# Optimization experiments

Hardware: AMD Instinct MI355X
Metric: run time of the kernel (lower is better)

Reference implementation:

```python
import jax, jax.numpy as jnp
import numpy as np

MODES = 16
WIDTH = 64
DEPTH = 4
MLP = 128


def spectral_conv(x, w_cplx):
    # x: [B, C, H, W] float32; w_cplx: [C, C, m1, m2] complex64
    B, C, H, W = x.shape
    x_ft = jnp.fft.rfft2(x)  # [B, C, H, W//2+1] complex
    m1, m2 = MODES, MODES
    low = jnp.einsum('bixy,ioxy->boxy', x_ft[:, :, :m1, :m2], w_cplx)
    out_ft = jnp.zeros((B, C, H, W // 2 + 1), dtype=jnp.complex64)
    out_ft = out_ft.at[:, :, :m1, :m2].set(low)
    return jnp.fft.irfft2(out_ft, s=(H, W)).astype(x.dtype)


def conv1x1(x, w, b):
    # x: [B,Cin,H,W], w: [Cout,Cin], b: [Cout]
    return jnp.einsum('bihw,oi->bohw', x, w) + b[None, :, None, None]


def setup_inputs() -> dict:
    key = jax.random.key(0)
    ks = jax.random.split(key, 4 + 4 * DEPTH)
    inp = {}
    inp['x'] = jax.random.normal(ks[0], (8, 3, 256, 256), dtype=jnp.float32)
    inp['fc0_w'] = jax.random.normal(ks[1], (WIDTH, 3), dtype=jnp.float32) * 0.1
    inp['fc0_b'] = jnp.zeros((WIDTH,), dtype=jnp.float32)
    scale = 1.0 / (WIDTH * WIDTH)
    sw_re, sw_im, ww, wb = [], [], [], []
    for i in range(DEPTH):
        k1, k2, k3 = jax.random.split(ks[4 + i], 3)
        sw_re.append(scale * jax.random.uniform(k1, (WIDTH, WIDTH, MODES, MODES), dtype=jnp.float32))
        sw_im.append(scale * jax.random.uniform(k2, (WIDTH, WIDTH, MODES, MODES), dtype=jnp.float32))
        ww.append(jax.random.normal(k3, (WIDTH, WIDTH), dtype=jnp.float32) * 0.05)
        wb.append(jnp.zeros((WIDTH,), dtype=jnp.float32))
    inp['spec_w_re'] = jnp.stack(sw_re)  # [D, C, C, m1, m2]
    inp['spec_w_im'] = jnp.stack(sw_im)
    inp['w_w'] = jnp.stack(ww)           # [D, C, C]
    inp['w_b'] = jnp.stack(wb)           # [D, C]
    inp['fc1_w'] = jax.random.normal(ks[2], (MLP, WIDTH), dtype=jnp.float32) * 0.05
    inp['fc1_b'] = jnp.zeros((MLP,), dtype=jnp.float32)
    inp['fc2_w'] = jax.random.normal(ks[3], (3, MLP), dtype=jnp.float32) * 0.05
    inp['fc2_b'] = jnp.zeros((3,), dtype=jnp.float32)
    return inp


def reference(x, fc0_w, fc0_b, spec_w_re, spec_w_im, w_w, w_b, fc1_w, fc1_b, fc2_w, fc2_b):
    # Dropout is identity in eval mode.
    h = conv1x1(x, fc0_w, fc0_b)  # [B, WIDTH, H, W]
    for i in range(DEPTH):
        w_cplx = spec_w_re[i] + 1j * spec_w_im[i]
        x1 = spectral_conv(h, w_cplx)
        x2 = conv1x1(h, w_w[i], w_b[i])
        h = jax.nn.relu(x1 + x2)
    h = jnp.transpose(h, (0, 2, 3, 1))  # [B, H, W, WIDTH]
    h = jax.nn.relu(jnp.einsum('bhwc,mc->bhwm', h, fc1_w) + fc1_b)
    h = jnp.einsum('bhwm,om->bhwo', h, fc2_w) + fc2_b
    return jnp.transpose(h, (0, 3, 1, 2))  # [B, 3, H, W]
```

## Files before the change

### kernel.cpp

```cpp
#include <hip/hip_runtime.h>

#define Hd 256
#define Wd 256
#define HW 65536
#define C 64
#define B 8
#define M 16
#define NDEPTH 4
#define NMLP 128

typedef __attribute__((ext_vector_type(8))) __bf16 bf16x8;
typedef __attribute__((ext_vector_type(4))) float f32x4;

__device__ inline void bar_lgkm() {
    asm volatile("s_waitcnt lgkmcnt(0)" ::: "memory");
    __builtin_amdgcn_s_barrier();
}

__device__ inline void split_pack8(const float* v, uint4& hq, uint4& lq) {
    unsigned hw[4], lw[4];
#pragma unroll
    for (int i = 0; i < 4; ++i) {
        float a = v[2 * i], bb = v[2 * i + 1];
        unsigned ua = __float_as_uint(a);
        unsigned ha = (ua + 0x7fffu + ((ua >> 16) & 1u)) & 0xffff0000u;
        float ra = a - __uint_as_float(ha);
        unsigned ural = __float_as_uint(ra);
        unsigned la = (ural + 0x7fffu + ((ural >> 16) & 1u)) >> 16;
        unsigned ub = __float_as_uint(bb);
        unsigned hb = (ub + 0x7fffu + ((ub >> 16) & 1u)) & 0xffff0000u;
        float rb = bb - __uint_as_float(hb);
        unsigned urbl = __float_as_uint(rb);
        unsigned lb = (urbl + 0x7fffu + ((urbl >> 16) & 1u)) >> 16;
        hw[i] = (ha >> 16) | (hb & 0xffff0000u);
        lw[i] = la | (lb << 16);
    }
    hq = make_uint4(hw[0], hw[1], hw[2], hw[3]);
    lq = make_uint4(lw[0], lw[1], lw[2], lw[3]);
}

__device__ inline void split1(float s, ushort& h, ushort& l) {
    unsigned ua = __float_as_uint(s);
    unsigned ha = (ua + 0x7fffu + ((ua >> 16) & 1u)) & 0xffff0000u;
    float r = s - __uint_as_float(ha);
    unsigned ur = __float_as_uint(r);
    h = (ushort)(ha >> 16);
    l = (ushort)((ur + 0x7fffu + ((ur >> 16) & 1u)) >> 16);
}

__device__ inline uint4 pack8(const unsigned* v) {
    uint4 r;
    r.x = v[0] | (v[1] << 16);
    r.y = v[2] | (v[3] << 16);
    r.z = v[4] | (v[5] << 16);
    r.w = v[6] | (v[7] << 16);
    return r;
}


__global__ void k_table(float2* __restrict__ tab) {
    int t = threadIdx.x;
    double a = (6.283185307179586476925286766559 / 256.0) * (double)t;
    tab[t] = make_float2((float)cos(a), (float)sin(a));
}

__global__ void k_prep0(const float2* __restrict__ tab, const float* __restrict__ fc1w,
                        const float* __restrict__ ww, float* __restrict__ trig,
                        uint4* __restrict__ trigs_h, uint4* __restrict__ trigs_l,
                        uint4* __restrict__ wws_h, uint4* __restrict__ wws_l,
                        uint4* __restrict__ w1s_h, uint4* __restrict__ w1s_l) {
    int blk = blockIdx.x, t = threadIdx.x;
    if (blk < 32) {
        int k = blk & 15;
        float2 e = tab[(k * t) & 255];
        trig[blk * 256 + t] = (blk < 16) ? e.x : e.y;
    } else if (blk < 36) {
        int idx = (blk - 32) * 256 + t;
        int kc = idx >> 8, x = idx & 255;
        float v[8];
#pragma unroll
        for (int j = 0; j < 8; ++j) {
            int row = kc * 8 + j;
            float2 e = tab[((row & 15) * x) & 255];
            v[j] = (row < 16) ? e.x : e.y;
        }
        uint4 hq, lq; split_pack8(v, hq, lq);
        trigs_h[idx] = hq; trigs_l[idx] = lq;
    } else if (blk < 44) {
        int idx = (blk - 36) * 256 + t;
        int o = idx & 63, kc = (idx >> 6) & 3, ph = (idx >> 8) & 1, d = idx >> 9;
        float v[8];
#pragma unroll
        for (int j = 0; j < 8; ++j)
            v[j] = ww[d * 4096 + o * 64 + ph * 32 + kc * 8 + j];
        uint4 hq, lq; split_pack8(v, hq, lq);
        wws_h[idx] = hq; wws_l[idx] = lq;
    } else {
        int idx = (blk - 44) * 256 + t;
        int m = idx & 127, kc = (idx >> 7) & 3, ph = idx >> 9;
        float v[8];
#pragma unroll
        for (int j = 0; j < 8; ++j)
            v[j] = fc1w[m * 64 + ph * 32 + kc * 8 + j];
        uint4 hq, lq; split_pack8(v, hq, lq);
        w1s_h[idx] = hq; w1s_l[idx] = lq;
    }
}

__global__ void k_prep_et(const float2* __restrict__ tab,
                          uint4* __restrict__ ETh, uint4* __restrict__ ETl) {
    int c = blockIdx.x * 256 + threadIdx.x;
    if (c >= 1024) return;
    int ph = c >> 7, kc = (c >> 5) & 3, m = c & 31;
    float v[8];
#pragma unroll
    for (int j = 0; j < 8; ++j) {
        int y = ph * 32 + kc * 8 + j;
        float2 e = tab[((m & 15) * y) & 255];
        v[j] = (m < 16) ? e.x : -e.y;
    }
    uint4 hq, lq;
    split_pack8(v, hq, lq);
    ETh[c] = hq; ETl[c] = lq;
}

__global__ void k_fc0(const float* __restrict__ x, const float* __restrict__ w,
                      const float* __restrict__ bias,
                      ushort* __restrict__ hs_h, ushort* __restrict__ hs_l) {
    int gp = blockIdx.x * 256 + threadIdx.x;
    int b = gp >> 13, pg = gp & 8191;
    int pix0 = pg * 8;
    float xv[3][8];
#pragma unroll
    for (int ch = 0; ch < 3; ++ch) {
        float4 a = *(const float4*)(x + (size_t)(b * 3 + ch) * HW + pix0);
        float4 c4 = *(const float4*)(x + (size_t)(b * 3 + ch) * HW + pix0 + 4);
        xv[ch][0] = a.x; xv[ch][1] = a.y; xv[ch][2] = a.z; xv[ch][3] = a.w;
        xv[ch][4] = c4.x; xv[ch][5] = c4.y; xv[ch][6] = c4.z; xv[ch][7] = c4.w;
    }
    for (int o = 0; o < C; ++o) {
        float w0 = w[o * 3 + 0], w1 = w[o * 3 + 1], w2 = w[o * 3 + 2], bv = bias[o];
        float v[8];
#pragma unroll
        for (int j = 0; j < 8; ++j)
            v[j] = fmaf(w0, xv[0][j], fmaf(w1, xv[1][j], fmaf(w2, xv[2][j], bv)));
        uint4 hq, lq; split_pack8(v, hq, lq);
        *(uint4*)(hs_h + (size_t)(b * 64 + o) * HW + pix0) = hq;
        *(uint4*)(hs_l + (size_t)(b * 64 + o) * HW + pix0) = lq;
    }
}

__global__ __launch_bounds__(256, 4)
void k_fwd_y(const ushort* __restrict__ hs_h, const ushort* __restrict__ hs_l,
             const uint4* __restrict__ ETh, const uint4* __restrict__ ETl,
             float* __restrict__ T1F) {
    int blk = blockIdx.x;
    int xh = blk & 1, bc = blk >> 1;
    int x0 = xh * 128;
    int t = threadIdx.x;
    int w = t >> 6, l = t & 63;
    int lr = l & 15, lq = l >> 4;
    const ushort* pH = hs_h + (size_t)bc * HW + x0 + w * 32 + lr;
    const ushort* pL = hs_l + (size_t)bc * HW + x0 + w * 32 + lr;
    f32x4 acc[2][2];
#pragma unroll
    for (int u = 0; u < 2; ++u)
#pragma unroll
        for (int xt = 0; xt < 2; ++xt) {
            acc[u][xt][0] = 0.f; acc[u][xt][1] = 0.f;
            acc[u][xt][2] = 0.f; acc[u][xt][3] = 0.f;
        }
    unsigned h0[2][8], l0[2][8], h1[2][8], l1[2][8];
    auto loadp = [&](unsigned hv[2][8], unsigned lv[2][8], int ph) {
#pragma unroll
        for (int xt = 0; xt < 2; ++xt)
#pragma unroll
            for (int j = 0; j < 8; ++j) {
                int off = (ph * 32 + lq * 8 + j) * 256 + xt * 16;
                hv[xt][j] = pH[off];
                lv[xt][j] = pL[off];
            }
    };
    loadp(h0, l0, 0);
#pragma unroll
    for (int ph = 0; ph < 8; ++ph) {
        unsigned (*ch)[8] = (ph & 1) ? h1 : h0;
        unsigned (*cl)[8] = (ph & 1) ? l1 : l0;
        unsigned (*nh)[8] = (ph & 1) ? h0 : h1;
        unsigned (*nl)[8] = (ph & 1) ? l0 : l1;
        if (ph < 7) loadp(nh, nl, ph + 1);
        bf16x8 Ah[2], Al[2];
#pragma unroll
        for (int u = 0; u < 2; ++u) {
            int ci = ph * 128 + lq * 32 + u * 16 + lr;
            Ah[u] = __builtin_bit_cast(bf16x8, ETh[ci]);
            Al[u] = __builtin_bit_cast(bf16x8, ETl[ci]);
        }
#pragma unroll
        for (int xt = 0; xt < 2; ++xt) {
            bf16x8 Bh = __builtin_bit_cast(bf16x8, pack8(ch[xt]));
            bf16x8 Bl = __builtin_bit_cast(bf16x8, pack8(cl[xt]));
#pragma unroll
            for (int u = 0; u < 2; ++u) {
                acc[u][xt] = __builtin_amdgcn_mfma_f32_16x16x32_bf16(Ah[u], Bh, acc[u][xt], 0, 0, 0);
                acc[u][xt] = __builtin_amdgcn_mfma_f32_16x16x32_bf16(Ah[u], Bl, acc[u][xt], 0, 0, 0);
                acc[u][xt] = __builtin_amdgcn_mfma_f32_16x16x32_bf16(Al[u], Bh, acc[u][xt], 0, 0, 0);
            }
        }
    }
#pragma unroll
    for (int u = 0; u < 2; ++u)
#pragma unroll
        for (int xt = 0; xt < 2; ++xt)
#pragma unroll
            for (int g = 0; g < 4; ++g)
                T1F[(size_t)bc * 8192 + (u * 16 + lq * 4 + g) * 256 + x0 + w * 32 + xt * 16 + lr] =
                    acc[u][xt][g];
}

__global__ __launch_bounds__(256, 2)
void k_fwd_x(const float* __restrict__ T1F, const float* __restrict__ trig,
             float2* __restrict__ X) {
    __shared__ float sT[32 * 260];
    __shared__ float sG[32 * 260];
    int bc = blockIdx.x, t = threadIdx.x;
#pragma unroll
    for (int p = 0; p < 8; ++p) {
        int f = t + p * 256;
        int row = f >> 6, seg = f & 63;
        ((float4*)(sT + row * 260))[seg] = *(const float4*)(T1F + (size_t)bc * 8192 + f * 4);
        ((float4*)(sG + row * 260))[seg] = *(const float4*)(trig + row * 256 + seg * 4);
    }
    __syncthreads();
    int ky = t >> 4, kx = t & 15;
    const float* Tr = sT + ky * 260;
    const float* Ti = sT + (16 + ky) * 260;
    const float* Cs = sG + kx * 260;
    const float* Sn = sG + (16 + kx) * 260;
    float xr0 = 0.f, xi0 = 0.f, xr1 = 0.f, xi1 = 0.f;
    for (int q = 0; q < 64; q += 2) {
        float4 tr = *(const float4*)(Tr + q * 4);
        float4 ti = *(const float4*)(Ti + q * 4);
        float4 cs = *(const float4*)(Cs + q * 4);
        float4 sn = *(const float4*)(Sn + q * 4);
        xr0 = fmaf(tr.x, cs.x, xr0); xr0 = fmaf(ti.x, sn.x, xr0);
        xi0 = fmaf(ti.x, cs.x, xi0); xi0 = fmaf(-tr.x, sn.x, xi0);
        xr0 = fmaf(tr.y, cs.y, xr0); xr0 = fmaf(ti.y, sn.y, xr0);
        xi0 = fmaf(ti.y, cs.y, xi0); xi0 = fmaf(-tr.y, sn.y, xi0);
        xr0 = fmaf(tr.z, cs.z, xr0); xr0 = fmaf(ti.z, sn.z, xr0);
        xi0 = fmaf(ti.z, cs.z, xi0); xi0 = fmaf(-tr.z, sn.z, xi0);
        xr0 = fmaf(tr.w, cs.w, xr0); xr0 = fmaf(ti.w, sn.w, xr0);
        xi0 = fmaf(ti.w, cs.w, xi0); xi0 = fmaf(-tr.w, sn.w, xi0);
        float4 tr1 = *(const float4*)(Tr + q * 4 + 4);
        float4 ti1 = *(const float4*)(Ti + q * 4 + 4);
        float4 cs1 = *(const float4*)(Cs + q * 4 + 4);
        float4 sn1 = *(const float4*)(Sn + q * 4 + 4);
        xr1 = fmaf(tr1.x, cs1.x, xr1); xr1 = fmaf(ti1.x, sn1.x, xr1);
        xi1 = fmaf(ti1.x, cs1.x, xi1); xi1 = fmaf(-tr1.x, sn1.x, xi1);
        xr1 = fmaf(tr1.y, cs1.y, xr1); xr1 = fmaf(ti1.y, sn1.y, xr1);
        xi1 = fmaf(ti1.y, cs1.y, xi1); xi1 = fmaf(-tr1.y, sn1.y, xi1);
        xr1 = fmaf(tr1.z, cs1.z, xr1); xr1 = fmaf(ti1.z, sn1.z, xr1);
        xi1 = fmaf(ti1.z, cs1.z, xi1); xi1 = fmaf(-tr1.z, sn1.z, xi1);
        xr1 = fmaf(tr1.w, cs1.w, xr1); xr1 = fmaf(ti1.w, sn1.w, xr1);
        xi1 = fmaf(ti1.w, cs1.w, xi1); xi1 = fmaf(-tr1.w, sn1.w, xi1);
    }
    X[bc * 256 + t] = make_float2(xr0 + xr1, xi0 + xi1);
}

__global__ __launch_bounds__(256, 2)
void k_mix(const float2* __restrict__ X, const float* __restrict__ wre,
           const float* __restrict__ wim, float2* __restrict__ Y) {
    int o = blockIdx.x >> 2;
    int bq = blockIdx.x & 3;
    int m = threadIdx.x;
    int b0 = bq * 2, b1 = bq * 2 + 1;
    float yr0 = 0.f, yi0 = 0.f, yr1 = 0.f, yi1 = 0.f;
    for (int i = 0; i < C; ++i) {
        float wr = wre[(i * C + o) * 256 + m];
        float wi = wim[(i * C + o) * 256 + m];
        float2 x0 = X[(b0 * C + i) * 256 + m];
        float2 x1 = X[(b1 * C + i) * 256 + m];
        yr0 = fmaf(x0.x, wr, fmaf(-x0.y, wi, yr0));
        yi0 = fmaf(x0.x, wi, fmaf(x0.y, wr, yi0));
        yr1 = fmaf(x1.x, wr, fmaf(-x1.y, wi, yr1));
        yi1 = fmaf(x1.x, wi, fmaf(x1.y, wr, yi1));
    }
    Y[(b0 * C + o) * 256 + m] = make_float2(yr0, yi0);
    Y[(b1 * C + o) * 256 + m] = make_float2(yr1, yi1);
}

__global__ __launch_bounds__(256, 2)
void k_invy(const float2* __restrict__ Y, const float2* __restrict__ tab,
            float* __restrict__ Gq) {
    __shared__ float2 st[256];
    int blk = blockIdx.x;
    int yt = blk & 15, pg = (blk >> 4) & 3, b = blk >> 6;
    int t = threadIdx.x;
    st[t] = tab[t];
    int o = t & 63, kx = pg * 4 + (t >> 6);
    __syncthreads();
    float sc = (kx == 0 ? 1.0f : 2.0f) * (1.0f / 65536.0f);
    float yr[16], yi[16];
    const float2* yp = Y + (size_t)(b * 64 + o) * 256 + kx;
#pragma unroll
    for (int ky = 0; ky < 16; ++ky) {
        float2 v = yp[ky * 16];
        yr[ky] = v.x * sc;
        yi[ky] = v.y * sc;
    }
    int y0 = yt * 16;
    for (int yy = 0; yy < 16; ++yy) {
        int y = y0 + yy;
        float re = 0.f, im = 0.f;
#pragma unroll
        for (int ky = 0; ky < 16; ++ky) {
            float2 e = st[(ky * y) & 255];
            re = fmaf(yr[ky], e.x, re);
            re = fmaf(-yi[ky], e.y, re);
            im = fmaf(yr[ky], e.y, im);
            im = fmaf(yi[ky], e.x, im);
        }
        float* gp = Gq + (size_t)(b * 256 + y) * 32 * 64 + o;
        gp[kx * 64] = re;
        gp[(16 + kx) * 64] = -im;
    }
}

__global__ __launch_bounds__(256, 4)
void k_final(ushort* __restrict__ hs_h, ushort* __restrict__ hs_l,
             const float* __restrict__ Gq,
             const uint4* __restrict__ wws_h, const uint4* __restrict__ wws_l,
             const float* __restrict__ wb,
             const uint4* __restrict__ trigs_h, const uint4* __restrict__ trigs_l) {
    __shared__ uint4 smem[2560];
    uint4* sH0h = smem;
    uint4* sH0l = smem + 512;
    uint4* sH1h = smem + 1024;
    uint4* sH1l = smem + 1536;
    uint4* sGh  = smem + 2048;
    uint4* sGl  = smem + 2304;
    int blk = blockIdx.x;
    int xq = blk & 1, y = (blk >> 1) & 255, b = blk >> 9;
    int x0 = xq * 128;
    int t = threadIdx.x;
    int os = t & 63, q = t >> 6;
    int w = t >> 6, l = t & 63;
    int lr = l & 15, lq = l >> 4;
    int xs = t & 127, half = t >> 7;
    f32x4 acc[8];
    {
        int ob = w * 16 + lq * 4;
        f32x4 ini;
        ini[0] = wb[ob]; ini[1] = wb[ob + 1]; ini[2] = wb[ob + 2]; ini[3] = wb[ob + 3];
#pragma unroll
        for (int xt = 0; xt < 8; ++xt) acc[xt] = ini;
    }
    float gv[8];
    {
        const float* gsrc = Gq + ((size_t)(b * 256 + y) * 32 + q * 8) * 64 + os;
#pragma unroll
        for (int kk = 0; kk < 8; ++kk) gv[kk] = gsrc[kk * 64];
    }
    uint4 A0h = wws_h[lq * 64 + w * 16 + lr];
    uint4 A0l = wws_l[lq * 64 + w * 16 + lr];
    uint4 A1h = wws_h[(4 + lq) * 64 + w * 16 + lr];
    uint4 A1l = wws_l[(4 + lq) * 64 + w * 16 + lr];
    size_t hb0 = (size_t)(b * 64 + half * 16) * HW + y * 256 + x0 + xs;
    unsigned hv[16], lv[16];
#pragma unroll
    for (int j = 0; j < 16; ++j) {
        hv[j] = hs_h[hb0 + (size_t)j * HW];
        lv[j] = hs_l[hb0 + (size_t)j * HW];
    }
    {
        uint4 ghq, glq; split_pack8(gv, ghq, glq);
        sGh[q * 64 + os] = ghq; sGl[q * 64 + os] = glq;
    }
#pragma unroll
    for (int c2 = 0; c2 < 2; ++c2) {
        int cell = (half * 2 + c2) * 128 + xs;
        sH0h[cell] = pack8(hv + c2 * 8);
        sH0l[cell] = pack8(lv + c2 * 8);
    }
    unsigned hv1[16], lv1[16];
    size_t hb1 = hb0 + (size_t)32 * HW;
#pragma unroll
    for (int j = 0; j < 16; ++j) {
        hv1[j] = hs_h[hb1 + (size_t)j * HW];
        lv1[j] = hs_l[hb1 + (size_t)j * HW];
    }
    bar_lgkm();
#pragma unroll
    for (int xt = 0; xt < 8; ++xt) {
        bf16x8 Bh = __builtin_bit_cast(bf16x8, sH0h[lq * 128 + xt * 16 + lr]);
        bf16x8 Bl = __builtin_bit_cast(bf16x8, sH0l[lq * 128 + xt * 16 + lr]);
        bf16x8 Ah = __builtin_bit_cast(bf16x8, A0h);
        bf16x8 Al = __builtin_bit_cast(bf16x8, A0l);
        acc[xt] = __builtin_amdgcn_mfma_f32_16x16x32_bf16(Ah, Bh, acc[xt], 0, 0, 0);
        acc[xt] = __builtin_amdgcn_mfma_f32_16x16x32_bf16(Ah, Bl, acc[xt], 0, 0, 0);
        acc[xt] = __builtin_amdgcn_mfma_f32_16x16x32_bf16(Al, Bh, acc[xt], 0, 0, 0);
    }
#pragma unroll
    for (int c2 = 0; c2 < 2; ++c2) {
        int cell = (half * 2 + c2) * 128 + xs;
        sH1h[cell] = pack8(hv1 + c2 * 8);
        sH1l[cell] = pack8(lv1 + c2 * 8);
    }
    bar_lgkm();
#pragma unroll
    for (int xt = 0; xt < 8; ++xt) {
        bf16x8 Bh = __builtin_bit_cast(bf16x8, sH1h[lq * 128 + xt * 16 + lr]);
        bf16x8 Bl = __builtin_bit_cast(bf16x8, sH1l[lq * 128 + xt * 16 + lr]);
        bf16x8 Ah = __builtin_bit_cast(bf16x8, A1h);
        bf16x8 Al = __builtin_bit_cast(bf16x8, A1l);
        acc[xt] = __builtin_amdgcn_mfma_f32_16x16x32_bf16(Ah, Bh, acc[xt], 0, 0, 0);
        acc[xt] = __builtin_amdgcn_mfma_f32_16x16x32_bf16(Ah, Bl, acc[xt], 0, 0, 0);
        acc[xt] = __builtin_amdgcn_mfma_f32_16x16x32_bf16(Al, Bh, acc[xt], 0, 0, 0);
    }
    {
        bf16x8 Ah = __builtin_bit_cast(bf16x8, sGh[lq * 64 + w * 16 + lr]);
        bf16x8 Al = __builtin_bit_cast(bf16x8, sGl[lq * 64 + w * 16 + lr]);
#pragma unroll
        for (int xt = 0; xt < 8; ++xt) {
            bf16x8 Bh = __builtin_bit_cast(bf16x8, trigs_h[lq * 256 + x0 + xt * 16 + lr]);
            bf16x8 Bl = __builtin_bit_cast(bf16x8, trigs_l[lq * 256 + x0 + xt * 16 + lr]);
            acc[xt] = __builtin_amdgcn_mfma_f32_16x16x32_bf16(Ah, Bh, acc[xt], 0, 0, 0);
            acc[xt] = __builtin_amdgcn_mfma_f32_16x16x32_bf16(Ah, Bl, acc[xt], 0, 0, 0);
            acc[xt] = __builtin_amdgcn_mfma_f32_16x16x32_bf16(Al, Bh, acc[xt], 0, 0, 0);
        }
    }
    __syncthreads();
    ushort* eh = (ushort*)smem;
    ushort* el = (ushort*)(smem + 1024);
    int swz = lq * 40;
#pragma unroll
    for (int xt = 0; xt < 8; ++xt)
#pragma unroll
        for (int g = 0; g < 4; ++g) {
            int o = w * 16 + lq * 4 + g;
            float r = fmaxf(acc[xt][g], 0.f);
            ushort hh, ll; split1(r, hh, ll);
            int col = (xt * 16 + lr) ^ swz;
            eh[o * 128 + col] = hh;
            el[o * 128 + col] = ll;
        }
    __syncthreads();
#pragma unroll
    for (int p = 0; p < 4; ++p) {
        int f = t + p * 256;
        int o = f >> 4, seg = f & 15;
        int ko = ((o >> 2) & 3) * 40;
        int cb = (seg * 8) ^ ko;
        size_t base = (size_t)(b * 64 + o) * HW + y * 256 + x0;
        *(uint4*)(hs_h + base + seg * 8) = *(uint4*)(eh + o * 128 + cb);
        *(uint4*)(hs_l + base + seg * 8) = *(uint4*)(el + o * 128 + cb);
    }
}

__global__ __launch_bounds__(256, 3)
void k_final_fc(const ushort* __restrict__ hs_h, const ushort* __restrict__ hs_l,
                const float* __restrict__ Gq,
                const uint4* __restrict__ wws_h, const uint4* __restrict__ wws_l,
                const float* __restrict__ wb,
                const uint4* __restrict__ trigs_h, const uint4* __restrict__ trigs_l,
                const uint4* __restrict__ w1s_h, const uint4* __restrict__ w1s_l,
                const float* __restrict__ b1, const float* __restrict__ w2,
                const float* __restrict__ b2, float* __restrict__ out) {
    __shared__ uint4 smem[2048];
    uint4* sH0h = smem;
    uint4* sH0l = smem + 512;
    uint4* sH1h = smem + 1024;
    uint4* sH1l = smem + 1536;
    int blk = blockIdx.x;
    int xq = blk & 1, y = (blk >> 1) & 255, b = blk >> 9;
    int x0 = xq * 128;
    int t = threadIdx.x;
    int w = t >> 6, l = t & 63;
    int lr = l & 15, lq = l >> 4;
    int xs = t & 127, half = t >> 7;
    f32x4 acc[8];
    {
        int ob = w * 16 + lq * 4;
        f32x4 ini;
        ini[0] = wb[ob]; ini[1] = wb[ob + 1]; ini[2] = wb[ob + 2]; ini[3] = wb[ob + 3];
#pragma unroll
        for (int xt = 0; xt < 8; ++xt) acc[xt] = ini;
    }
    float gv[8];
    {
        const float* gsrc = Gq + ((size_t)(b * 256 + y) * 32 + lq * 8) * 64 + w * 16 + lr;
#pragma unroll
        for (int kk = 0; kk < 8; ++kk) gv[kk] = gsrc[kk * 64];
    }
    uint4 A0h = wws_h[lq * 64 + w * 16 + lr];
    uint4 A0l = wws_l[lq * 64 + w * 16 + lr];
    uint4 A1h = wws_h[(4 + lq) * 64 + w * 16 + lr];
    uint4 A1l = wws_l[(4 + lq) * 64 + w * 16 + lr];
    size_t hb0 = (size_t)(b * 64 + half * 16) * HW + y * 256 + x0 + xs;
    unsigned hv[16], lv[16];
#pragma unroll
    for (int j = 0; j < 16; ++j) {
        hv[j] = hs_h[hb0 + (size_t)j * HW];
        lv[j] = hs_l[hb0 + (size_t)j * HW];
    }
#pragma unroll
    for (int c2 = 0; c2 < 2; ++c2) {
        int cell = (half * 2 + c2) * 128 + xs;
        sH0h[cell] = pack8(hv + c2 * 8);
        sH0l[cell] = pack8(lv + c2 * 8);
    }
    unsigned hv1[16], lv1[16];
    size_t hb1 = hb0 + (size_t)32 * HW;
#pragma unroll
    for (int j = 0; j < 16; ++j) {
        hv1[j] = hs_h[hb1 + (size_t)j * HW];
        lv1[j] = hs_l[hb1 + (size_t)j * HW];
    }
    bar_lgkm();
#pragma unroll
    for (int xt = 0; xt < 8; ++xt) {
        bf16x8 Bh = __builtin_bit_cast(bf16x8, sH0h[lq * 128 + xt * 16 + lr]);
        bf16x8 Bl = __builtin_bit_cast(bf16x8, sH0l[lq * 128 + xt * 16 + lr]);
        bf16x8 Ah = __builtin_bit_cast(bf16x8, A0h);
        bf16x8 Al = __builtin_bit_cast(bf16x8, A0l);
        acc[xt] = __builtin_amdgcn_mfma_f32_16x16x32_bf16(Ah, Bh, acc[xt], 0, 0, 0);
        acc[xt] = __builtin_amdgcn_mfma_f32_16x16x32_bf16(Ah, Bl, acc[xt], 0, 0, 0);
        acc[xt] = __builtin_amdgcn_mfma_f32_16x16x32_bf16(Al, Bh, acc[xt], 0, 0, 0);
    }
#pragma unroll
    for (int c2 = 0; c2 < 2; ++c2) {
        int cell = (half * 2 + c2) * 128 + xs;
        sH1h[cell] = pack8(hv1 + c2 * 8);
        sH1l[cell] = pack8(lv1 + c2 * 8);
    }
    bar_lgkm();
#pragma unroll
    for (int xt = 0; xt < 8; ++xt) {
        bf16x8 Bh = __builtin_bit_cast(bf16x8, sH1h[lq * 128 + xt * 16 + lr]);
        bf16x8 Bl = __builtin_bit_cast(bf16x8, sH1l[lq * 128 + xt * 16 + lr]);
        bf16x8 Ah = __builtin_bit_cast(bf16x8, A1h);
        bf16x8 Al = __builtin_bit_cast(bf16x8, A1l);
        acc[xt] = __builtin_amdgcn_mfma_f32_16x16x32_bf16(Ah, Bh, acc[xt], 0, 0, 0);
        acc[xt] = __builtin_amdgcn_mfma_f32_16x16x32_bf16(Ah, Bl, acc[xt], 0, 0, 0);
        acc[xt] = __builtin_amdgcn_mfma_f32_16x16x32_bf16(Al, Bh, acc[xt], 0, 0, 0);
    }
    {
        uint4 gh4, gl4; split_pack8(gv, gh4, gl4);
        bf16x8 Ah = __builtin_bit_cast(bf16x8, gh4);
        bf16x8 Al = __builtin_bit_cast(bf16x8, gl4);
#pragma unroll
        for (int xt = 0; xt < 8; ++xt) {
            bf16x8 Bh = __builtin_bit_cast(bf16x8, trigs_h[lq * 256 + x0 + xt * 16 + lr]);
            bf16x8 Bl = __builtin_bit_cast(bf16x8, trigs_l[lq * 256 + x0 + xt * 16 + lr]);
            acc[xt] = __builtin_amdgcn_mfma_f32_16x16x32_bf16(Ah, Bh, acc[xt], 0, 0, 0);
            acc[xt] = __builtin_amdgcn_mfma_f32_16x16x32_bf16(Ah, Bl, acc[xt], 0, 0, 0);
            acc[xt] = __builtin_amdgcn_mfma_f32_16x16x32_bf16(Al, Bh, acc[xt], 0, 0, 0);
        }
    }
    __syncthreads();
    ushort* ch16 = (ushort*)smem;
    ushort* cl16 = (ushort*)(smem + 1024);
#pragma unroll
    for (int xt = 0; xt < 8; ++xt)
#pragma unroll
        for (int g = 0; g < 4; ++g) {
            int o = w * 16 + lq * 4 + g;
            float r = fmaxf(acc[xt][g], 0.f);
            ushort hh, ll; split1(r, hh, ll);
            int ci = ((o >> 3) * 128 + xt * 16 + lr) * 8 + (o & 7);
            ch16[ci] = hh;
            cl16[ci] = ll;
        }
    __syncthreads();
    uint4* cells_h = smem;
    uint4* cells_l = smem + 1024;
    int mb = w * 32;
    f32x4 acc2[2][8];
#pragma unroll
    for (int u = 0; u < 2; ++u) {
        int m0 = mb + u * 16 + lq * 4;
        f32x4 ini;
        ini[0] = b1[m0]; ini[1] = b1[m0 + 1]; ini[2] = b1[m0 + 2]; ini[3] = b1[m0 + 3];
#pragma unroll
        for (int xt = 0; xt < 8; ++xt) acc2[u][xt] = ini;
    }
#pragma unroll
    for (int ph = 0; ph < 2; ++ph) {
        bf16x8 Ah[2], Al[2];
#pragma unroll
        for (int u = 0; u < 2; ++u) {
            Ah[u] = __builtin_bit_cast(bf16x8, w1s_h[(ph * 4 + lq) * 128 + mb + u * 16 + lr]);
            Al[u] = __builtin_bit_cast(bf16x8, w1s_l[(ph * 4 + lq) * 128 + mb + u * 16 + lr]);
        }
#pragma unroll
        for (int xt = 0; xt < 8; ++xt) {
            bf16x8 Bh = __builtin_bit_cast(bf16x8, cells_h[(ph * 4 + lq) * 128 + xt * 16 + lr]);
            bf16x8 Bl = __builtin_bit_cast(bf16x8, cells_l[(ph * 4 + lq) * 128 + xt * 16 + lr]);
#pragma unroll
            for (int u = 0; u < 2; ++u) {
                acc2[u][xt] = __builtin_amdgcn_mfma_f32_16x16x32_bf16(Ah[u], Bh, acc2[u][xt], 0, 0, 0);
                acc2[u][xt] = __builtin_amdgcn_mfma_f32_16x16x32_bf16(Ah[u], Bl, acc2[u][xt], 0, 0, 0);
                acc2[u][xt] = __builtin_amdgcn_mfma_f32_16x16x32_bf16(Al[u], Bh, acc2[u][xt], 0, 0, 0);
            }
        }
    }
    float pj[3][8];
#pragma unroll
    for (int j = 0; j < 3; ++j)
#pragma unroll
        for (int xt = 0; xt < 8; ++xt) pj[j][xt] = 0.f;
#pragma unroll
    for (int u = 0; u < 2; ++u)
#pragma unroll
        for (int g = 0; g < 4; ++g) {
            int m = mb + u * 16 + lq * 4 + g;
            float w20 = w2[m], w21 = w2[NMLP + m], w22 = w2[2 * NMLP + m];
#pragma unroll
            for (int xt = 0; xt < 8; ++xt) {
                float r = fmaxf(acc2[u][xt][g], 0.f);
                pj[0][xt] = fmaf(w20, r, pj[0][xt]);
                pj[1][xt] = fmaf(w21, r, pj[1][xt]);
                pj[2][xt] = fmaf(w22, r, pj[2][xt]);
            }
        }
#pragma unroll
    for (int j = 0; j < 3; ++j)
#pragma unroll
        for (int xt = 0; xt < 8; ++xt) {
            float v = pj[j][xt];
            v += __shfl_xor(v, 16);
            v += __shfl_xor(v, 32);
            pj[j][xt] = v;
        }
    __syncthreads();
    float* part = (float*)smem;
    if (lq == 0) {
#pragma unroll
        for (int j = 0; j < 3; ++j)
#pragma unroll
            for (int xt = 0; xt < 8; ++xt)
                part[(w * 3 + j) * 128 + xt * 16 + lr] = pj[j][xt];
    }
    __syncthreads();
#pragma unroll
    for (int r = 0; r < 2; ++r) {
        int idx = t + r * 256;
        if (idx < 384) {
            int j = idx >> 7, xx = idx & 127;
            float s = b2[j];
#pragma unroll
            for (int ww2 = 0; ww2 < 4; ++ww2) s += part[(ww2 * 3 + j) * 128 + xx];
            out[(size_t)(b * 3 + j) * HW + y * 256 + x0 + xx] = s;
        }
    }
}

extern "C" void kernel_launch(void* const* d_in, const int* in_sizes, int n_in,
                              void* d_out, int out_size, void* d_ws, size_t ws_size,
                              hipStream_t stream) {
    const float* x     = (const float*)d_in[0];
    const float* fc0_w = (const float*)d_in[1];
    const float* fc0_b = (const float*)d_in[2];
    const float* swre  = (const float*)d_in[3];
    const float* swim  = (const float*)d_in[4];
    const float* ww    = (const float*)d_in[5];
    const float* wb    = (const float*)d_in[6];
    const float* fc1w  = (const float*)d_in[7];
    const float* fc1b  = (const float*)d_in[8];
    const float* fc2w  = (const float*)d_in[9];
    const float* fc2b  = (const float*)d_in[10];

    float* ws = (float*)d_ws;
    float2* tab     = (float2*)ws;
    ushort* hs_h    = (ushort*)(ws + 512);
    ushort* hs_l    = (ushort*)(ws + 512 + 16777216);
    float*  T1F     = ws + 33554944;
    float2* X       = (float2*)(ws + 37749248);
    float2* Y       = (float2*)(ws + 38011392);
    float*  Gq      = ws + 38273536;
    float*  trig    = ws + 42467840;
    uint4*  trigs_h = (uint4*)(ws + 42476032);
    uint4*  trigs_l = (uint4*)(ws + 42480128);
    uint4*  wws_h   = (uint4*)(ws + 42484224);
    uint4*  wws_l   = (uint4*)(ws + 42492416);
    uint4*  w1s_h   = (uint4*)(ws + 42500608);
    uint4*  w1s_l   = (uint4*)(ws + 42504704);
    uint4*  ETh     = (uint4*)(ws + 42508800);
    uint4*  ETl     = (uint4*)(ws + 42512896);

    k_table<<<dim3(1), dim3(256), 0, stream>>>(tab);
    k_prep0<<<dim3(48), dim3(256), 0, stream>>>(tab, fc1w, ww, trig,
                                                trigs_h, trigs_l, wws_h, wws_l,
                                                w1s_h, w1s_l);
    k_prep_et<<<dim3(4), dim3(256), 0, stream>>>(tab, ETh, ETl);
    k_fc0<<<dim3(256), dim3(256), 0, stream>>>(x, fc0_w, fc0_b, hs_h, hs_l);

    for (int d = 0; d < NDEPTH; ++d) {
        k_fwd_y<<<dim3(1024), dim3(256), 0, stream>>>(hs_h, hs_l, ETh, ETl, T1F);
        k_fwd_x<<<dim3(512), dim3(256), 0, stream>>>(T1F, trig, X);
        k_mix<<<dim3(256), dim3(256), 0, stream>>>(X, swre + (size_t)d * C * C * 256,
                                                   swim + (size_t)d * C * C * 256, Y);
        k_invy<<<dim3(512), dim3(256), 0, stream>>>(Y, tab, Gq);
        if (d < NDEPTH - 1) {
            k_final<<<dim3(4096), dim3(256), 0, stream>>>(hs_h, hs_l, Gq,
                                                          wws_h + (size_t)d * 512,
                                                          wws_l + (size_t)d * 512,
                                                          wb + d * C, trigs_h, trigs_l);
        } else {
            k_final_fc<<<dim3(4096), dim3(256), 0, stream>>>(hs_h, hs_l, Gq,
                                                             wws_h + (size_t)d * 512,
                                                             wws_l + (size_t)d * 512,
                                                             wb + d * C, trigs_h, trigs_l,
                                                             w1s_h, w1s_l, fc1b, fc2w,
                                                             fc2b, (float*)d_out);
        }
    }
}
```

Baseline: 654.7 us.

## Move x-direction forward DFT onto bf16-split MFMA with bf16 intermediate

The second forward DFT stage (along x) drops its scalar FP32 FMA loop and becomes a split-bf16 MFMA GEMM against a new precomputed twiddle table (TXh/TXl). k_fwd_y now stages its outputs through swizzled shared memory and writes them as hi/lo bf16 pairs instead of fp32, which halves the intermediate's bytes and provides the MFMA-ready layout. Two smaller changes ride along: k_final_fc gets a higher occupancy hint and packs its relu outputs into vectorized uint2 stores. The three-term split-bf16 product approximates fp32 and may introduce small precision differences.

```diff
diff --git a/kernel.cpp b/kernel.cpp
--- a/kernel.cpp
+++ b/kernel.cpp
@@ -108,20 +108,33 @@
 }
 
 __global__ void k_prep_et(const float2* __restrict__ tab,
-                          uint4* __restrict__ ETh, uint4* __restrict__ ETl) {
+                          uint4* __restrict__ ETh, uint4* __restrict__ ETl,
+                          uint4* __restrict__ TXh, uint4* __restrict__ TXl) {
     int c = blockIdx.x * 256 + threadIdx.x;
-    if (c >= 1024) return;
-    int ph = c >> 7, kc = (c >> 5) & 3, m = c & 31;
-    float v[8];
-#pragma unroll
-    for (int j = 0; j < 8; ++j) {
-        int y = ph * 32 + kc * 8 + j;
-        float2 e = tab[((m & 15) * y) & 255];
-        v[j] = (m < 16) ? e.x : -e.y;
-    }
-    uint4 hq, lq;
-    split_pack8(v, hq, lq);
-    ETh[c] = hq; ETl[c] = lq;
+    if (c < 1024) {
+        int ph = c >> 7, kc = (c >> 5) & 3, m = c & 31;
+        float v[8];
+#pragma unroll
+        for (int j = 0; j < 8; ++j) {
+            int y = ph * 32 + kc * 8 + j;
+            float2 e = tab[((m & 15) * y) & 255];
+            v[j] = (m < 16) ? e.x : -e.y;
+        }
+        uint4 hq, lq; split_pack8(v, hq, lq);
+        ETh[c] = hq; ETl[c] = lq;
+    } else if (c < 2048) {
+        int cc = c - 1024;
+        int kcq = cc >> 5, km = cc & 31;
+        float v[8];
+#pragma unroll
+        for (int j = 0; j < 8; ++j) {
+            int x = kcq * 8 + j;
+            float2 e = tab[((km & 15) * x) & 255];
+            v[j] = (km < 16) ? e.x : e.y;
+        }
+        uint4 hq, lq; split_pack8(v, hq, lq);
+        TXh[cc] = hq; TXl[cc] = lq;
+    }
 }
 
 __global__ void k_fc0(const float* __restrict__ x, const float* __restrict__ w,
@@ -153,7 +166,8 @@
 __global__ __launch_bounds__(256, 4)
 void k_fwd_y(const ushort* __restrict__ hs_h, const ushort* __restrict__ hs_l,
              const uint4* __restrict__ ETh, const uint4* __restrict__ ETl,
-             float* __restrict__ T1F) {
+             ushort* __restrict__ T1Fs_h, ushort* __restrict__ T1Fs_l) {
+    __shared__ ushort eh[32 * 128], el[32 * 128];
     int blk = blockIdx.x;
     int xh = blk & 1, bc = blk >> 1;
     int x0 = xh * 128;
@@ -208,63 +222,65 @@
             }
         }
     }
+    int swz = lq * 40;
 #pragma unroll
     for (int u = 0; u < 2; ++u)
 #pragma unroll
         for (int xt = 0; xt < 2; ++xt)
 #pragma unroll
-            for (int g = 0; g < 4; ++g)
-                T1F[(size_t)bc * 8192 + (u * 16 + lq * 4 + g) * 256 + x0 + w * 32 + xt * 16 + lr] =
-                    acc[u][xt][g];
-}
-
-__global__ __launch_bounds__(256, 2)
-void k_fwd_x(const float* __restrict__ T1F, const float* __restrict__ trig,
-             float2* __restrict__ X) {
-    __shared__ float sT[32 * 260];
-    __shared__ float sG[32 * 260];
-    int bc = blockIdx.x, t = threadIdx.x;
-#pragma unroll
-    for (int p = 0; p < 8; ++p) {
+            for (int g = 0; g < 4; ++g) {
+                int row = u * 16 + lq * 4 + g;
+                int col = (w * 32 + xt * 16 + lr) ^ swz;
+                ushort hh, ll; split1(acc[u][xt][g], hh, ll);
+                eh[row * 128 + col] = hh;
+                el[row * 128 + col] = ll;
+            }
+    __syncthreads();
+#pragma unroll
+    for (int p = 0; p < 2; ++p) {
         int f = t + p * 256;
-        int row = f >> 6, seg = f & 63;
-        ((float4*)(sT + row * 260))[seg] = *(const float4*)(T1F + (size_t)bc * 8192 + f * 4);
-        ((float4*)(sG + row * 260))[seg] = *(const float4*)(trig + row * 256 + seg * 4);
-    }
+        int row = f >> 4, seg = f & 15;
+        int cb = (seg * 8) ^ (((row >> 2) & 3) * 40);
+        size_t dst = (size_t)bc * 8192 + row * 256 + x0 + seg * 8;
+        *(uint4*)(T1Fs_h + dst) = *(uint4*)(eh + row * 128 + cb);
+        *(uint4*)(T1Fs_l + dst) = *(uint4*)(el + row * 128 + cb);
+    }
+}
+
+__global__ __launch_bounds__(256, 8)
+void k_fwd_x2(const ushort* __restrict__ T1Fs_h, const ushort* __restrict__ T1Fs_l,
+              const uint4* __restrict__ TXh, const uint4* __restrict__ TXl,
+              float2* __restrict__ X) {
+    __shared__ float sD[32 * 33];
+    int bc = blockIdx.x;
+    int t = threadIdx.x;
+    int w = t >> 6, l = t & 63;
+    int lr = l & 15, lq = l >> 4;
+    int u = w >> 1, v = w & 1;
+    f32x4 acc;
+    acc[0] = 0.f; acc[1] = 0.f; acc[2] = 0.f; acc[3] = 0.f;
+    const uint4* Ah4 = (const uint4*)T1Fs_h + ((size_t)bc * 32 + u * 16 + lr) * 32 + lq;
+    const uint4* Al4 = (const uint4*)T1Fs_l + ((size_t)bc * 32 + u * 16 + lr) * 32 + lq;
+    const uint4* Bh4 = TXh + lq * 32 + v * 16 + lr;
+    const uint4* Bl4 = TXl + lq * 32 + v * 16 + lr;
+#pragma unroll
+    for (int ph = 0; ph < 8; ++ph) {
+        bf16x8 Ah = __builtin_bit_cast(bf16x8, Ah4[ph * 4]);
+        bf16x8 Al = __builtin_bit_cast(bf16x8, Al4[ph * 4]);
+        bf16x8 Bh = __builtin_bit_cast(bf16x8, Bh4[ph * 128]);
+        bf16x8 Bl = __builtin_bit_cast(bf16x8, Bl4[ph * 128]);
+        acc = __builtin_amdgcn_mfma_f32_16x16x32_bf16(Ah, Bh, acc, 0, 0, 0);
+        acc = __builtin_amdgcn_mfma_f32_16x16x32_bf16(Ah, Bl, acc, 0, 0, 0);
+        acc = __builtin_amdgcn_mfma_f32_16x16x32_bf16(Al, Bh, acc, 0, 0, 0);
+    }
+#pragma unroll
+    for (int g = 0; g < 4; ++g)
+        sD[(u * 16 + lq * 4 + g) * 33 + v * 16 + lr] = acc[g];
     __syncthreads();
     int ky = t >> 4, kx = t & 15;
-    const float* Tr = sT + ky * 260;
-    const float* Ti = sT + (16 + ky) * 260;
-    const float* Cs = sG + kx * 260;
-    const float* Sn = sG + (16 + kx) * 260;
-    float xr0 = 0.f, xi0 = 0.f, xr1 = 0.f, xi1 = 0.f;
-    for (int q = 0; q < 64; q += 2) {
-        float4 tr = *(const float4*)(Tr + q * 4);
-        float4 ti = *(const float4*)(Ti + q * 4);
-        float4 cs = *(const float4*)(Cs + q * 4);
-        float4 sn = *(const float4*)(Sn + q * 4);
-        xr0 = fmaf(tr.x, cs.x, xr0); xr0 = fmaf(ti.x, sn.x, xr0);
-        xi0 = fmaf(ti.x, cs.x, xi0); xi0 = fmaf(-tr.x, sn.x, xi0);
-        xr0 = fmaf(tr.y, cs.y, xr0); xr0 = fmaf(ti.y, sn.y, xr0);
-        xi0 = fmaf(ti.y, cs.y, xi0); xi0 = fmaf(-tr.y, sn.y, xi0);
-        xr0 = fmaf(tr.z, cs.z, xr0); xr0 = fmaf(ti.z, sn.z, xr0);
-        xi0 = fmaf(ti.z, cs.z, xi0); xi0 = fmaf(-tr.z, sn.z, xi0);
-        xr0 = fmaf(tr.w, cs.w, xr0); xr0 = fmaf(ti.w, sn.w, xr0);
-        xi0 = fmaf(ti.w, cs.w, xi0); xi0 = fmaf(-tr.w, sn.w, xi0);
-        float4 tr1 = *(const float4*)(Tr + q * 4 + 4);
-        float4 ti1 = *(const float4*)(Ti + q * 4 + 4);
-        float4 cs1 = *(const float4*)(Cs + q * 4 + 4);
-        float4 sn1 = *(const float4*)(Sn + q * 4 + 4);
-        xr1 = fmaf(tr1.x, cs1.x, xr1); xr1 = fmaf(ti1.x, sn1.x, xr1);
-        xi1 = fmaf(ti1.x, cs1.x, xi1); xi1 = fmaf(-tr1.x, sn1.x, xi1);
-        xr1 = fmaf(tr1.y, cs1.y, xr1); xr1 = fmaf(ti1.y, sn1.y, xr1);
-        xi1 = fmaf(ti1.y, cs1.y, xi1); xi1 = fmaf(-tr1.y, sn1.y, xi1);
-        xr1 = fmaf(tr1.z, cs1.z, xr1); xr1 = fmaf(ti1.z, sn1.z, xr1);
-        xi1 = fmaf(ti1.z, cs1.z, xi1); xi1 = fmaf(-tr1.z, sn1.z, xi1);
-        xr1 = fmaf(tr1.w, cs1.w, xr1); xr1 = fmaf(ti1.w, sn1.w, xr1);
-        xi1 = fmaf(ti1.w, cs1.w, xi1); xi1 = fmaf(-tr1.w, sn1.w, xi1);
-    }
-    X[bc * 256 + t] = make_float2(xr0 + xr1, xi0 + xi1);
+    float xr = sD[ky * 33 + kx] + sD[(16 + ky) * 33 + 16 + kx];
+    float xi = sD[(16 + ky) * 33 + kx] - sD[ky * 33 + 16 + kx];
+    X[(size_t)bc * 256 + t] = make_float2(xr, xi);
 }
 
 __global__ __launch_bounds__(256, 2)
@@ -457,7 +473,7 @@
     }
 }
 
-__global__ __launch_bounds__(256, 3)
+__global__ __launch_bounds__(256, 4)
 void k_final_fc(const ushort* __restrict__ hs_h, const ushort* __restrict__ hs_l,
                 const float* __restrict__ Gq,
                 const uint4* __restrict__ wws_h, const uint4* __restrict__ wws_l,
@@ -560,17 +576,24 @@
     __syncthreads();
     ushort* ch16 = (ushort*)smem;
     ushort* cl16 = (ushort*)(smem + 1024);
-#pragma unroll
-    for (int xt = 0; xt < 8; ++xt)
-#pragma unroll
-        for (int g = 0; g < 4; ++g) {
-            int o = w * 16 + lq * 4 + g;
-            float r = fmaxf(acc[xt][g], 0.f);
-            ushort hh, ll; split1(r, hh, ll);
-            int ci = ((o >> 3) * 128 + xt * 16 + lr) * 8 + (o & 7);
-            ch16[ci] = hh;
-            cl16[ci] = ll;
-        }
+    {
+        int kcw = w * 2 + (lq >> 1);
+        int sb = (lq & 1) * 4;
+#pragma unroll
+        for (int xt = 0; xt < 8; ++xt) {
+            ushort hh[4], ll[4];
+#pragma unroll
+            for (int g = 0; g < 4; ++g) {
+                float r = fmaxf(acc[xt][g], 0.f);
+                split1(r, hh[g], ll[g]);
+            }
+            int ci = (kcw * 128 + xt * 16 + lr) * 8 + sb;
+            *(uint2*)(ch16 + ci) = make_uint2(hh[0] | ((unsigned)hh[1] << 16),
+                                              hh[2] | ((unsigned)hh[3] << 16));
+            *(uint2*)(cl16 + ci) = make_uint2(ll[0] | ((unsigned)ll[1] << 16),
+                                              ll[2] | ((unsigned)ll[3] << 16));
+        }
+    }
     __syncthreads();
     uint4* cells_h = smem;
     uint4* cells_l = smem + 1024;
@@ -674,7 +697,8 @@
     float2* tab     = (float2*)ws;
     ushort* hs_h    = (ushort*)(ws + 512);
     ushort* hs_l    = (ushort*)(ws + 512 + 16777216);
-    float*  T1F     = ws + 33554944;
+    ushort* T1Fs_h  = (ushort*)(ws + 33554944);
+    ushort* T1Fs_l  = (ushort*)(ws + 33554944 + 2097152);
     float2* X       = (float2*)(ws + 37749248);
     float2* Y       = (float2*)(ws + 38011392);
     float*  Gq      = ws + 38273536;
@@ -687,17 +711,20 @@
     uint4*  w1s_l   = (uint4*)(ws + 42504704);
     uint4*  ETh     = (uint4*)(ws + 42508800);
     uint4*  ETl     = (uint4*)(ws + 42512896);
+    uint4*  TXh     = (uint4*)(ws + 42516992);
+    uint4*  TXl     = (uint4*)(ws + 42521088);
 
     k_table<<<dim3(1), dim3(256), 0, stream>>>(tab);
     k_prep0<<<dim3(48), dim3(256), 0, stream>>>(tab, fc1w, ww, trig,
                                                 trigs_h, trigs_l, wws_h, wws_l,
                                                 w1s_h, w1s_l);
-    k_prep_et<<<dim3(4), dim3(256), 0, stream>>>(tab, ETh, ETl);
+    k_prep_et<<<dim3(8), dim3(256), 0, stream>>>(tab, ETh, ETl, TXh, TXl);
     k_fc0<<<dim3(256), dim3(256), 0, stream>>>(x, fc0_w, fc0_b, hs_h, hs_l);
 
     for (int d = 0; d < NDEPTH; ++d) {
-        k_fwd_y<<<dim3(1024), dim3(256), 0, stream>>>(hs_h, hs_l, ETh, ETl, T1F);
-        k_fwd_x<<<dim3(512), dim3(256), 0, stream>>>(T1F, trig, X);
+        k_fwd_y<<<dim3(1024), dim3(256), 0, stream>>>(hs_h, hs_l, ETh, ETl,
+                                                      T1Fs_h, T1Fs_l);
+        k_fwd_x2<<<dim3(512), dim3(256), 0, stream>>>(T1Fs_h, T1Fs_l, TXh, TXl, X);
         k_mix<<<dim3(256), dim3(256), 0, stream>>>(X, swre + (size_t)d * C * C * 256,
                                                    swim + (size_t)d * C * C * 256, Y);
         k_invy<<<dim3(512), dim3(256), 0, stream>>>(Y, tab, Gq);
```

Result: faster. 628.2 us (-4.0%).
